# Kernel tuning notes

Measured on AMD Instinct MI355X. Metric: run time of the kernel, lower is better.

## Reference

```python
import jax, jax.numpy as jnp
import numpy as np

N = 20000      # nodes
E = 50000      # edges
B = 128        # graphs in batch
H = 64         # hidden_dim
FEAT = 28      # raw node feature dim
N_TYPES = 100  # one-hot size for node_type
EDGE_DIM = 5   # one-hot size for edge_type
OUT = 1        # output_dim
MP_ITER = 3
S2S_ITER = 4


def setup_inputs() -> dict:
    key = jax.random.key(0)
    ks = jax.random.split(key, 24)
    s = 0.05
    inp = {
        'node_feat': jax.random.normal(ks[0], (N, FEAT), dtype=jnp.float32),
        'node_type': jax.random.randint(ks[1], (N,), 0, N_TYPES),
        'edge_index': jax.random.randint(ks[2], (2, E), 0, N),
        'edge_type': jax.random.randint(ks[3], (E,), 0, EDGE_DIM),
        'batch': jnp.sort(jax.random.randint(ks[4], (N,), 0, B)),
        # node embedding
        'W_emb': jax.random.normal(ks[5], (N_TYPES + FEAT, H), dtype=jnp.float32) * s,
        'b_emb': jnp.zeros((H,), dtype=jnp.float32),
        # shared edge net: edge_dim -> H -> H*H
        'W_e1': jax.random.normal(ks[6], (EDGE_DIM, H), dtype=jnp.float32) * s,
        'b_e1': jnp.zeros((H,), dtype=jnp.float32),
        'W_e2': jax.random.normal(ks[7], (H, H * H), dtype=jnp.float32) * s,
        'b_e2': jnp.zeros((H * H,), dtype=jnp.float32),
        # per-layer NNConv root weight + bias
        'roots': jax.random.normal(ks[8], (MP_ITER, H, H), dtype=jnp.float32) * s,
        'conv_bias': jnp.zeros((MP_ITER, H), dtype=jnp.float32),
        # Set2Set LSTM (input 2H, hidden H); torch gate order i,f,g,o
        'W_ih': jax.random.normal(ks[9], (4 * H, 2 * H), dtype=jnp.float32) * s,
        'W_hh': jax.random.normal(ks[10], (4 * H, H), dtype=jnp.float32) * s,
        'b_ih': jnp.zeros((4 * H,), dtype=jnp.float32),
        'b_hh': jnp.zeros((4 * H,), dtype=jnp.float32),
        # output MLP 2H -> H -> OUT
        'W_o1': jax.random.normal(ks[11], (2 * H, H), dtype=jnp.float32) * s,
        'b_o1': jnp.zeros((H,), dtype=jnp.float32),
        'W_o2': jax.random.normal(ks[12], (H, OUT), dtype=jnp.float32) * s,
        'b_o2': jnp.zeros((OUT,), dtype=jnp.float32),
    }
    return inp


def _forward(node_feat, W_emb, b_emb, W_e1, b_e1, W_e2, b_e2, roots, conv_bias,
             W_ih, W_hh, b_ih, b_hh, W_o1, b_o1, W_o2, b_o2,
             node_type, edge_index, edge_type, batch):
    # node embedding: [one_hot(node_type,100) ; node_feat] @ W_emb
    x_in = jnp.concatenate(
        [jax.nn.one_hot(node_type, N_TYPES, dtype=node_feat.dtype), node_feat], axis=-1)
    h = x_in @ W_emb + b_emb                                   # [N, H]

    # edge-conditioned weights (edge_attr is fixed, edge_net is shared across
    # iterations, so nn(edge_attr) is identical each layer -> compute once)
    edge_attr = jax.nn.one_hot(edge_type, EDGE_DIM, dtype=node_feat.dtype)
    Wmat = jax.nn.relu(edge_attr @ W_e1 + b_e1) @ W_e2 + b_e2  # [E, H*H]
    Wmat = Wmat.reshape(E, H, H)                               # [E, H_in, H_out]

    src, dst = edge_index[0], edge_index[1]
    for i in range(MP_ITER):
        msg = jnp.einsum('eh,eho->eo', h[src], Wmat)           # per-edge matvec
        agg = jax.ops.segment_sum(msg, dst, num_segments=N)    # sum aggregation
        h = agg + h @ roots[i] + conv_bias[i]                  # NNConv root + bias

    # Set2Set pooling
    hx = jnp.zeros((B, H), dtype=h.dtype)
    cx = jnp.zeros((B, H), dtype=h.dtype)
    q_star = jnp.zeros((B, 2 * H), dtype=h.dtype)
    for _ in range(S2S_ITER):
        gates = q_star @ W_ih.T + b_ih + hx @ W_hh.T + b_hh
        ig, fg, gg, og = jnp.split(gates, 4, axis=-1)
        cx = jax.nn.sigmoid(fg) * cx + jax.nn.sigmoid(ig) * jnp.tanh(gg)
        hx = jax.nn.sigmoid(og) * jnp.tanh(cx)
        q = hx                                                 # [B, H]
        e = jnp.sum(h * q[batch], axis=-1)                     # [N]
        m = jax.lax.stop_gradient(jax.ops.segment_max(e, batch, num_segments=B))
        a = jnp.exp(e - m[batch])
        denom = jax.ops.segment_sum(a, batch, num_segments=B)
        denom = jnp.where(denom == 0, 1.0, denom)
        a = a / denom[batch]                                   # scatter softmax
        r = jax.ops.segment_sum(a[:, None] * h, batch, num_segments=B)  # [B, H]
        q_star = jnp.concatenate([q, r], axis=-1)

    out = jax.nn.relu(q_star @ W_o1 + b_o1) @ W_o2 + b_o2      # [B, OUT]
    return out


def reference(node_feat, node_type, edge_index, edge_type, batch,
              W_emb, b_emb, W_e1, b_e1, W_e2, b_e2, roots, conv_bias,
              W_ih, W_hh, b_ih, b_hh, W_o1, b_o1, W_o2, b_o2):
    return _forward(node_feat, W_emb, b_emb, W_e1, b_e1, W_e2, b_e2, roots,
                    conv_bias, W_ih, W_hh, b_ih, b_hh, W_o1, b_o1, W_o2, b_o2,
                    node_type, edge_index, edge_type, batch)
```

## Files before the change

### kernel.cpp

```cpp
#include <hip/hip_runtime.h>
#include <math.h>


#define NN 20000
#define NE 50000
#define NB 128
#define HD 64
#define NFEAT 28
#define NTYPES 100
#define EDIM 5
#define MPIT 3
#define S2SIT 4
#define NBLK_E ((NE + 255) / 256)
#define SMAX 224
#define HP (HD + 1)

__device__ __forceinline__ float sigm(float x) {
  return 1.0f / (1.0f + expf(-x));
}

__global__ __launch_bounds__(256) void k_starts(
    const int* __restrict__ batch, int* __restrict__ gstart) {
  int n = blockIdx.x * blockDim.x + threadIdx.x;
  if (n >= NN) return;
  int b = batch[n];
  if (n == 0)
    for (int t = 0; t <= b; ++t) gstart[t] = 0;
  int bn = (n + 1 < NN) ? batch[n + 1] : NB;
  for (int t = b + 1; t <= bn; ++t) gstart[t] = n + 1;
}

__global__ __launch_bounds__(256) void k_setup(
    const float* __restrict__ feat, const int* __restrict__ ntype,
    const int* __restrict__ etype,
    const float* __restrict__ W_emb, const float* __restrict__ b_emb,
    const float* __restrict__ W_e1, const float* __restrict__ b_e1,
    const float* __restrict__ W_e2, const float* __restrict__ b_e2,
    const float* __restrict__ W_ih, const float* __restrict__ W_hh,
    float* __restrict__ Wty, float* __restrict__ hA, float* __restrict__ hB,
    float* __restrict__ W_ihT, float* __restrict__ W_hhT,
    int* __restrict__ bc) {
  __shared__ int wcc[4][EDIM];
  __shared__ float sv[EDIM][HD];
  __shared__ float red[4][EDIM][HD];
  const int tid = threadIdx.x;
  const int lane = tid & 63;
  const int wv = tid >> 6;
  const int blk = blockIdx.x;
  const int nblk = gridDim.x;
  const int nthr = nblk << 8;
  const int gtid = (blk << 8) + tid;
  const int gw = (blk << 2) + wv;
  const int nwave = nblk << 2;

  if (blk < NBLK_E) {
    int e = (blk << 8) + tid;
    int ty = (e < NE) ? etype[e] : -1;
    #pragma unroll
    for (int t = 0; t < EDIM; ++t) {
      unsigned long long m = __ballot(ty == t);
      if (lane == 0) wcc[wv][t] = __popcll(m);
    }
    __syncthreads();
    if (tid < EDIM)
      bc[blk * EDIM + tid] = wcc[0][tid] + wcc[1][tid] + wcc[2][tid] + wcc[3][tid];
    __syncthreads();
  }

  if (blk >= NBLK_E && blk < NBLK_E + 64) {
    int mbase = (blk - NBLK_E) * 64;
    for (int idx = tid; idx < EDIM * HD; idx += 256) {
      int t = idx >> 6, j = idx & 63;
      float x = W_e1[t * HD + j] + b_e1[j];
      sv[t][j] = x > 0.f ? x : 0.f;
    }
    __syncthreads();
    int l = tid & 63, jg = tid >> 6;
    float acc[EDIM] = {0.f, 0.f, 0.f, 0.f, 0.f};
    #pragma unroll
    for (int jj = 0; jj < 16; ++jj) {
      int j = jg * 16 + jj;
      float w2 = W_e2[j * 4096 + mbase + l];
      #pragma unroll
      for (int t = 0; t < EDIM; ++t) acc[t] = fmaf(sv[t][j], w2, acc[t]);
    }
    #pragma unroll
    for (int t = 0; t < EDIM; ++t) red[jg][t][l] = acc[t];
    __syncthreads();
    for (int idx = tid; idx < EDIM * HD; idx += 256) {
      int t = idx >> 6, m = idx & 63;
      float s = red[0][t][m] + red[1][t][m] + red[2][t][m] + red[3][t][m];
      Wty[t * 4096 + mbase + m] = s + b_e2[mbase + m];
    }
  }

  for (int o = gtid; o < 2 * HD * 4 * HD; o += nthr)
    W_ihT[o] = W_ih[(o & 255) * 128 + (o >> 8)];
  for (int o = gtid; o < HD * 4 * HD; o += nthr)
    W_hhT[o] = W_hh[(o & 255) * 64 + (o >> 8)];

  {
    float wf[NFEAT];
    #pragma unroll
    for (int f = 0; f < NFEAT; ++f) wf[f] = W_emb[(NTYPES + f) * HD + lane];
    float bb = b_emb[lane];
    for (int n = gw; n < NN; n += nwave) {
      int nu = __builtin_amdgcn_readfirstlane(n);
      int t = __builtin_amdgcn_readfirstlane(ntype[nu]);
      const float* row = feat + nu * NFEAT;
      float acc = bb + W_emb[t * HD + lane];
      #pragma unroll
      for (int f = 0; f < NFEAT; ++f) acc = fmaf(row[f], wf[f], acc);
      hA[nu * HD + lane] = acc;
    }
  }

  {
    float4 z = make_float4(0.f, 0.f, 0.f, 0.f);
    for (int i = gtid; i < NN * HD / 4; i += nthr)
      reinterpret_cast<float4*>(hB)[i] = z;
  }
}

__global__ __launch_bounds__(256) void k_place(
    const int* __restrict__ etype, const int* __restrict__ ei,
    const int* __restrict__ bc,
    int* __restrict__ srcs, int* __restrict__ dsts, int* __restrict__ offs_out) {
  __shared__ int s_base[EDIM];
  __shared__ int wc[4][EDIM];
  const int tid = threadIdx.x;
  const int lane = tid & 63;
  const int wv = tid >> 6;
  const int blk = blockIdx.x;

  if (wv == 0) {
    int part[EDIM], tot[EDIM];
    #pragma unroll
    for (int t = 0; t < EDIM; ++t) { part[t] = 0; tot[t] = 0; }
    for (int b = lane; b < NBLK_E; b += 64) {
      #pragma unroll
      for (int t = 0; t < EDIM; ++t) {
        int x = bc[b * EDIM + t];
        tot[t] += x;
        if (b < blk) part[t] += x;
      }
    }
    #pragma unroll
    for (int t = 0; t < EDIM; ++t) {
      #pragma unroll
      for (int off = 32; off; off >>= 1) {
        tot[t]  += __shfl_xor(tot[t],  off, 64);
        part[t] += __shfl_xor(part[t], off, 64);
      }
    }
    if (lane == 0) {
      int run = 0;
      #pragma unroll
      for (int t = 0; t < EDIM; ++t) {
        s_base[t] = run + part[t];
        if (blk == 0) offs_out[t] = run;
        run += tot[t];
      }
      if (blk == 0) offs_out[EDIM] = run;
    }
  }

  int e = (blk << 8) + tid;
  int ty = (e < NE) ? etype[e] : -1;
  int sv = 0, dv = 0;
  if (e < NE) { sv = ei[e]; dv = ei[NE + e]; }
  int rank = 0;
  #pragma unroll
  for (int t = 0; t < EDIM; ++t) {
    unsigned long long m = __ballot(ty == t);
    if (lane == 0) wc[wv][t] = __popcll(m);
    if (ty == t) rank = __popcll(m & ((1ull << lane) - 1ull));
  }
  __syncthreads();
  if (ty >= 0) {
    int base = s_base[ty];
    for (int w = 0; w < wv; ++w) base += wc[w][ty];
    srcs[base + rank] = sv;
    dsts[base + rank] = dv;
  }
}

__global__ __launch_bounds__(256) void k_mp(
    const int* __restrict__ srcs, const int* __restrict__ dsts,
    const int* __restrict__ offs_in,
    const float* __restrict__ Wty, const float* __restrict__ hsrc,
    float* __restrict__ htgt, float* __restrict__ hzero,
    const float* __restrict__ root, const float* __restrict__ bias) {
  const int lane = threadIdx.x & 63;
  const int wv = threadIdx.x >> 6;
  const int blk = blockIdx.x;

  if (blk < 512) {
    float w[HD];
    #pragma unroll
    for (int k = 0; k < HD; ++k) w[k] = root[k * HD + lane];
    float bb = bias[lane];
    int rw = (blk << 2) + wv;
    for (int n = rw; n < NN; n += 2048) {
      int nu = __builtin_amdgcn_readfirstlane(n);
      const float* row = hsrc + nu * HD;
      float a0 = bb, a1 = 0.f, a2 = 0.f, a3 = 0.f;
      #pragma unroll
      for (int k = 0; k < HD; k += 4) {
        a0 = fmaf(row[k + 0], w[k + 0], a0);
        a1 = fmaf(row[k + 1], w[k + 1], a1);
        a2 = fmaf(row[k + 2], w[k + 2], a2);
        a3 = fmaf(row[k + 3], w[k + 3], a3);
      }
      atomicAdd(&htgt[nu * HD + lane], (a0 + a1) + (a2 + a3));
    }
    if (hzero) {
      float4 z = make_float4(0.f, 0.f, 0.f, 0.f);
      for (int i = (blk << 8) + threadIdx.x; i < NN * HD / 4; i += 512 * 256)
        reinterpret_cast<float4*>(hzero)[i] = z;
    }
  } else {
    int wid = ((blk - 512) << 2) + wv;
    const int nw = 8192;
    int per = (NE + nw - 1) / nw;
    int beg = wid * per;
    int end = beg + per; if (end > NE) end = NE;
    if (beg >= end) return;
    int offs[EDIM + 1];
    #pragma unroll
    for (int t = 0; t <= EDIM; ++t) offs[t] = offs_in[t];
    for (int t = 0; t < EDIM; ++t) {
      int lo = offs[t];     if (lo < beg) lo = beg;
      int hi = offs[t + 1]; if (hi > end) hi = end;
      if (lo >= hi) continue;
      float w[HD];
      #pragma unroll
      for (int k = 0; k < HD; ++k) w[k] = Wty[t * 4096 + k * HD + lane];
      for (int p = lo; p < hi; ++p) {
        int s = __builtin_amdgcn_readfirstlane(srcs[p]);
        int d = __builtin_amdgcn_readfirstlane(dsts[p]);
        const float* row = hsrc + s * HD;
        float a0 = 0.f, a1 = 0.f, a2 = 0.f, a3 = 0.f;
        #pragma unroll
        for (int k = 0; k < HD; k += 4) {
          a0 = fmaf(row[k + 0], w[k + 0], a0);
          a1 = fmaf(row[k + 1], w[k + 1], a1);
          a2 = fmaf(row[k + 2], w[k + 2], a2);
          a3 = fmaf(row[k + 3], w[k + 3], a3);
        }
        atomicAdd(&htgt[d * HD + lane], (a0 + a1) + (a2 + a3));
      }
    }
  }
}

__global__ __launch_bounds__(256) void k_s2s(
    const float* __restrict__ h, const int* __restrict__ gstart,
    const float* __restrict__ W_ihT, const float* __restrict__ W_hhT,
    const float* __restrict__ b_ih, const float* __restrict__ b_hh,
    const float* __restrict__ W_o1, const float* __restrict__ b_o1,
    const float* __restrict__ W_o2, const float* __restrict__ b_o2,
    float* __restrict__ out) {
  __shared__ float hs[SMAX * HP];
  __shared__ float ebuf[SMAX];
  __shared__ float qstar[2 * HD];
  __shared__ float hxs[HD], cxs[HD], gates[4 * HD];
  __shared__ float redM[4], redS[4], redR[4][HD];
  __shared__ float hid[HD];
  int b = blockIdx.x;
  int tid = threadIdx.x;
  int lane = tid & 63, wv = tid >> 6;

  int st = gstart[b], en = gstart[b + 1];
  int cnt = en - st;
  int cached = cnt < SMAX ? cnt : SMAX;

  int total = cached * HD;
  for (int base = tid * 4; base < total; base += 1024) {
    float4 v = *reinterpret_cast<const float4*>(h + st * HD + base);
    int n = base >> 6, k = base & 63;
    float* row = hs + n * HP + k;
    row[0] = v.x; row[1] = v.y; row[2] = v.z; row[3] = v.w;
  }
  if (tid < 2 * HD) qstar[tid] = 0.f;
  if (tid < HD) { hxs[tid] = 0.f; cxs[tid] = 0.f; }
  __syncthreads();

  for (int it = 0; it < S2SIT; ++it) {
    float acc0 = b_ih[tid] + b_hh[tid], acc1 = 0.f;
    #pragma unroll 8
    for (int j = 0; j < 2 * HD; j += 2) {
      acc0 = fmaf(qstar[j],     W_ihT[j * 256 + tid],       acc0);
      acc1 = fmaf(qstar[j + 1], W_ihT[(j + 1) * 256 + tid], acc1);
    }
    #pragma unroll 8
    for (int j = 0; j < HD; j += 2) {
      acc0 = fmaf(hxs[j],     W_hhT[j * 256 + tid],       acc0);
      acc1 = fmaf(hxs[j + 1], W_hhT[(j + 1) * 256 + tid], acc1);
    }
    gates[tid] = acc0 + acc1;
    __syncthreads();
    if (tid < HD) {
      float ig = sigm(gates[tid]);
      float fg = sigm(gates[HD + tid]);
      float gg = tanhf(gates[2 * HD + tid]);
      float og = sigm(gates[3 * HD + tid]);
      float c = fmaf(fg, cxs[tid], ig * gg);
      cxs[tid] = c;
      hxs[tid] = og * tanhf(c);
    }
    __syncthreads();

    float e = -1e30f;
    if (tid < cached) {
      const float* row = hs + tid * HP;
      float d0 = 0.f, d1 = 0.f;
      #pragma unroll 8
      for (int k = 0; k < HD; k += 2) {
        d0 = fmaf(row[k],     hxs[k],     d0);
        d1 = fmaf(row[k + 1], hxs[k + 1], d1);
      }
      e = d0 + d1;
      ebuf[tid] = e;
    }
    float m = e;
    #pragma unroll
    for (int off = 32; off; off >>= 1) m = fmaxf(m, __shfl_xor(m, off, 64));
    float qreg = hxs[lane];
    for (int n = cached + wv; n < cnt; n += 4) {
      float ev = h[(st + n) * HD + lane] * qreg;
      #pragma unroll
      for (int off = 32; off; off >>= 1) ev += __shfl_xor(ev, off, 64);
      m = fmaxf(m, ev);
    }
    if (lane == 0) redM[wv] = m;
    __syncthreads();
    float M = fmaxf(fmaxf(redM[0], redM[1]), fmaxf(redM[2], redM[3]));

    float sp = 0.f;
    if (tid < cached) {
      float a = expf(ebuf[tid] - M);
      ebuf[tid] = a;
      sp = a;
    }
    #pragma unroll
    for (int off = 32; off; off >>= 1) sp += __shfl_xor(sp, off, 64);
    __syncthreads();

    float r = 0.f;
    for (int n = wv; n < cached; n += 4)
      r = fmaf(ebuf[n], hs[n * HP + lane], r);
    float s_tail = 0.f;
    for (int n = cached + wv; n < cnt; n += 4) {
      float v = h[(st + n) * HD + lane];
      float ev = v * qreg;
      #pragma unroll
      for (int off = 32; off; off >>= 1) ev += __shfl_xor(ev, off, 64);
      float a = expf(ev - M);
      s_tail += a;
      r = fmaf(a, v, r);
    }
    if (lane == 0) redS[wv] = sp + s_tail;
    redR[wv][lane] = r;
    __syncthreads();
    if (tid < HD) {
      float S = redS[0] + redS[1] + redS[2] + redS[3];
      float R = redR[0][tid] + redR[1][tid] + redR[2][tid] + redR[3][tid];
      if (S == 0.f) S = 1.f;
      qstar[tid] = hxs[tid];
      qstar[HD + tid] = R / S;
    }
    __syncthreads();
  }

  if (tid < HD) {
    float acc = b_o1[tid];
    #pragma unroll 8
    for (int i = 0; i < 2 * HD; ++i)
      acc = fmaf(qstar[i], W_o1[i * HD + tid], acc);
    hid[tid] = acc > 0.f ? acc : 0.f;
  }
  __syncthreads();
  if (tid < HD) {
    float p = hid[tid] * W_o2[tid];
    #pragma unroll
    for (int off = 32; off; off >>= 1) p += __shfl_xor(p, off, 64);
    if (tid == 0) out[b] = p + b_o2[0];
  }
}

extern "C" void kernel_launch(void* const* d_in, const int* in_sizes, int n_in,
                              void* d_out, int out_size, void* d_ws, size_t ws_size,
                              hipStream_t stream) {
  const float* node_feat = (const float*)d_in[0];
  const int*   node_type = (const int*)d_in[1];
  const int*   edge_index= (const int*)d_in[2];
  const int*   edge_type = (const int*)d_in[3];
  const int*   batch     = (const int*)d_in[4];
  const float* W_emb     = (const float*)d_in[5];
  const float* b_emb     = (const float*)d_in[6];
  const float* W_e1      = (const float*)d_in[7];
  const float* b_e1      = (const float*)d_in[8];
  const float* W_e2      = (const float*)d_in[9];
  const float* b_e2      = (const float*)d_in[10];
  const float* roots     = (const float*)d_in[11];
  const float* conv_bias = (const float*)d_in[12];
  const float* W_ih      = (const float*)d_in[13];
  const float* W_hh      = (const float*)d_in[14];
  const float* b_ih      = (const float*)d_in[15];
  const float* b_hh      = (const float*)d_in[16];
  const float* W_o1      = (const float*)d_in[17];
  const float* b_o1      = (const float*)d_in[18];
  const float* W_o2      = (const float*)d_in[19];
  const float* b_o2      = (const float*)d_in[20];
  float* out = (float*)d_out;

  float* Wty   = (float*)d_ws;
  float* hA    = Wty + EDIM * 4096;
  float* hB    = hA + NN * HD;
  float* hC    = hB + NN * HD;
  float* W_ihT = hC + NN * HD;
  float* W_hhT = W_ihT + 2 * HD * 4 * HD;
  int*   srcs  = (int*)(W_hhT + HD * 4 * HD);
  int*   dsts  = srcs + NE;
  int*   gstart= dsts + NE;
  int*   bc    = gstart + 136;
  int*   offs  = bc + NBLK_E * EDIM;

  k_starts<<<(NN + 255) / 256, 256, 0, stream>>>(batch, gstart);
  k_setup<<<512, 256, 0, stream>>>(node_feat, node_type, edge_type,
                                   W_emb, b_emb, W_e1, b_e1, W_e2, b_e2,
                                   W_ih, W_hh, Wty, hA, hB, W_ihT, W_hhT, bc);
  k_place<<<NBLK_E, 256, 0, stream>>>(edge_type, edge_index, bc, srcs, dsts, offs);

  k_mp<<<2560, 256, 0, stream>>>(srcs, dsts, offs, Wty, hA, hB, hC,
                                 roots + 0 * HD * HD, conv_bias + 0 * HD);
  k_mp<<<2560, 256, 0, stream>>>(srcs, dsts, offs, Wty, hB, hC, hA,
                                 roots + 1 * HD * HD, conv_bias + 1 * HD);
  k_mp<<<2560, 256, 0, stream>>>(srcs, dsts, offs, Wty, hC, hA, (float*)0,
                                 roots + 2 * HD * HD, conv_bias + 2 * HD);

  k_s2s<<<NB, 256, 0, stream>>>(hA, gstart, W_ihT, W_hhT, b_ih, b_hh,
                                W_o1, b_o1, W_o2, b_o2, out);
}
```

Measured before the change: 208.9 us.

## Split message passing into root-store and edge-atomic kernels, drop zero-fill buffer

Replaces the fused per-layer kernel with two launches per layer. The first is a root-transform kernel that writes bias plus h·root directly with plain stores. The second is an edge-message kernel that atomically accumulates into that same buffer. This removes the separate zero-fill passes and the third ping-pong buffer, avoids atomics on the root contribution, and packs src/dst into int2 for a single load per edge. In exchange there are three extra kernel launches, and the root and edge work are serialized within each layer instead of running concurrently.

```diff
diff --git a/kernel.cpp b/kernel.cpp
--- a/kernel.cpp
+++ b/kernel.cpp
@@ -37,7 +37,7 @@
     const float* __restrict__ W_e1, const float* __restrict__ b_e1,
     const float* __restrict__ W_e2, const float* __restrict__ b_e2,
     const float* __restrict__ W_ih, const float* __restrict__ W_hh,
-    float* __restrict__ Wty, float* __restrict__ hA, float* __restrict__ hB,
+    float* __restrict__ Wty, float* __restrict__ hA,
     float* __restrict__ W_ihT, float* __restrict__ W_hhT,
     int* __restrict__ bc) {
   __shared__ int wcc[4][EDIM];
@@ -114,18 +114,12 @@
       hA[nu * HD + lane] = acc;
     }
   }
-
-  {
-    float4 z = make_float4(0.f, 0.f, 0.f, 0.f);
-    for (int i = gtid; i < NN * HD / 4; i += nthr)
-      reinterpret_cast<float4*>(hB)[i] = z;
-  }
 }
 
 __global__ __launch_bounds__(256) void k_place(
     const int* __restrict__ etype, const int* __restrict__ ei,
     const int* __restrict__ bc,
-    int* __restrict__ srcs, int* __restrict__ dsts, int* __restrict__ offs_out) {
+    int2* __restrict__ sd, int* __restrict__ offs_out) {
   __shared__ int s_base[EDIM];
   __shared__ int wc[4][EDIM];
   const int tid = threadIdx.x;
@@ -180,31 +174,62 @@
   if (ty >= 0) {
     int base = s_base[ty];
     for (int w = 0; w < wv; ++w) base += wc[w][ty];
-    srcs[base + rank] = sv;
-    dsts[base + rank] = dv;
-  }
-}
-
-__global__ __launch_bounds__(256) void k_mp(
-    const int* __restrict__ srcs, const int* __restrict__ dsts,
-    const int* __restrict__ offs_in,
-    const float* __restrict__ Wty, const float* __restrict__ hsrc,
-    float* __restrict__ htgt, float* __restrict__ hzero,
+    sd[base + rank] = make_int2(sv, dv);
+  }
+}
+
+__global__ __launch_bounds__(256) void k_root(
+    const float* __restrict__ h, float* __restrict__ hnext,
     const float* __restrict__ root, const float* __restrict__ bias) {
   const int lane = threadIdx.x & 63;
+  const int wid = __builtin_amdgcn_readfirstlane(blockIdx.x * 4 + (threadIdx.x >> 6));
+  const int nw = gridDim.x * 4;
+  float w[HD];
+  #pragma unroll
+  for (int k = 0; k < HD; ++k) w[k] = root[k * HD + lane];
+  float bb = bias[lane];
+  for (int n = wid; n < NN; n += nw) {
+    const float* row = h + n * HD;
+    float a0 = 0.f, a1 = 0.f, a2 = 0.f, a3 = 0.f;
+    #pragma unroll
+    for (int k = 0; k < HD; k += 4) {
+      a0 = fmaf(row[k + 0], w[k + 0], a0);
+      a1 = fmaf(row[k + 1], w[k + 1], a1);
+      a2 = fmaf(row[k + 2], w[k + 2], a2);
+      a3 = fmaf(row[k + 3], w[k + 3], a3);
+    }
+    hnext[n * HD + lane] = bb + ((a0 + a1) + (a2 + a3));
+  }
+}
+
+__global__ __launch_bounds__(256) void k_msg(
+    const int2* __restrict__ sd, const int* __restrict__ offs_in,
+    const float* __restrict__ Wty, const float* __restrict__ hsrc,
+    float* __restrict__ htgt) {
+  const int lane = threadIdx.x & 63;
   const int wv = threadIdx.x >> 6;
-  const int blk = blockIdx.x;
-
-  if (blk < 512) {
+  int wid = (blockIdx.x << 2) + wv;
+  const int nw = 8192;
+  int per = (NE + nw - 1) / nw;
+  int beg = wid * per;
+  int end = beg + per; if (end > NE) end = NE;
+  if (beg >= end) return;
+  int offs[EDIM + 1];
+  #pragma unroll
+  for (int t = 0; t <= EDIM; ++t) offs[t] = offs_in[t];
+  for (int t = 0; t < EDIM; ++t) {
+    int lo = offs[t];     if (lo < beg) lo = beg;
+    int hi = offs[t + 1]; if (hi > end) hi = end;
+    if (lo >= hi) continue;
     float w[HD];
     #pragma unroll
-    for (int k = 0; k < HD; ++k) w[k] = root[k * HD + lane];
-    float bb = bias[lane];
-    int rw = (blk << 2) + wv;
-    for (int n = rw; n < NN; n += 2048) {
-      int nu = __builtin_amdgcn_readfirstlane(n);
-      const float* row = hsrc + nu * HD;
-      float a0 = bb, a1 = 0.f, a2 = 0.f, a3 = 0.f;
+    for (int k = 0; k < HD; ++k) w[k] = Wty[t * 4096 + k * HD + lane];
+    for (int p = lo; p < hi; ++p) {
+      int2 e = sd[p];
+      int s = __builtin_amdgcn_readfirstlane(e.x);
+      int d = __builtin_amdgcn_readfirstlane(e.y);
+      const float* row = hsrc + s * HD;
+      float a0 = 0.f, a1 = 0.f, a2 = 0.f, a3 = 0.f;
       #pragma unroll
       for (int k = 0; k < HD; k += 4) {
         a0 = fmaf(row[k + 0], w[k + 0], a0);
@@ -212,44 +237,7 @@
         a2 = fmaf(row[k + 2], w[k + 2], a2);
         a3 = fmaf(row[k + 3], w[k + 3], a3);
       }
-      atomicAdd(&htgt[nu * HD + lane], (a0 + a1) + (a2 + a3));
-    }
-    if (hzero) {
-      float4 z = make_float4(0.f, 0.f, 0.f, 0.f);
-      for (int i = (blk << 8) + threadIdx.x; i < NN * HD / 4; i += 512 * 256)
-        reinterpret_cast<float4*>(hzero)[i] = z;
-    }
-  } else {
-    int wid = ((blk - 512) << 2) + wv;
-    const int nw = 8192;
-    int per = (NE + nw - 1) / nw;
-    int beg = wid * per;
-    int end = beg + per; if (end > NE) end = NE;
-    if (beg >= end) return;
-    int offs[EDIM + 1];
-    #pragma unroll
-    for (int t = 0; t <= EDIM; ++t) offs[t] = offs_in[t];
-    for (int t = 0; t < EDIM; ++t) {
-      int lo = offs[t];     if (lo < beg) lo = beg;
-      int hi = offs[t + 1]; if (hi > end) hi = end;
-      if (lo >= hi) continue;
-      float w[HD];
-      #pragma unroll
-      for (int k = 0; k < HD; ++k) w[k] = Wty[t * 4096 + k * HD + lane];
-      for (int p = lo; p < hi; ++p) {
-        int s = __builtin_amdgcn_readfirstlane(srcs[p]);
-        int d = __builtin_amdgcn_readfirstlane(dsts[p]);
-        const float* row = hsrc + s * HD;
-        float a0 = 0.f, a1 = 0.f, a2 = 0.f, a3 = 0.f;
-        #pragma unroll
-        for (int k = 0; k < HD; k += 4) {
-          a0 = fmaf(row[k + 0], w[k + 0], a0);
-          a1 = fmaf(row[k + 1], w[k + 1], a1);
-          a2 = fmaf(row[k + 2], w[k + 2], a2);
-          a3 = fmaf(row[k + 3], w[k + 3], a3);
-        }
-        atomicAdd(&htgt[d * HD + lane], (a0 + a1) + (a2 + a3));
-      }
+      atomicAdd(&htgt[d * HD + lane], (a0 + a1) + (a2 + a3));
     }
   }
 }
@@ -418,28 +406,28 @@
   float* Wty   = (float*)d_ws;
   float* hA    = Wty + EDIM * 4096;
   float* hB    = hA + NN * HD;
-  float* hC    = hB + NN * HD;
-  float* W_ihT = hC + NN * HD;
+  float* W_ihT = hB + NN * HD;
   float* W_hhT = W_ihT + 2 * HD * 4 * HD;
-  int*   srcs  = (int*)(W_hhT + HD * 4 * HD);
-  int*   dsts  = srcs + NE;
-  int*   gstart= dsts + NE;
+  int2*  sd    = (int2*)(W_hhT + HD * 4 * HD);
+  int*   gstart= (int*)(sd + NE);
   int*   bc    = gstart + 136;
   int*   offs  = bc + NBLK_E * EDIM;
 
   k_starts<<<(NN + 255) / 256, 256, 0, stream>>>(batch, gstart);
   k_setup<<<512, 256, 0, stream>>>(node_feat, node_type, edge_type,
                                    W_emb, b_emb, W_e1, b_e1, W_e2, b_e2,
-                                   W_ih, W_hh, Wty, hA, hB, W_ihT, W_hhT, bc);
-  k_place<<<NBLK_E, 256, 0, stream>>>(edge_type, edge_index, bc, srcs, dsts, offs);
-
-  k_mp<<<2560, 256, 0, stream>>>(srcs, dsts, offs, Wty, hA, hB, hC,
-                                 roots + 0 * HD * HD, conv_bias + 0 * HD);
-  k_mp<<<2560, 256, 0, stream>>>(srcs, dsts, offs, Wty, hB, hC, hA,
-                                 roots + 1 * HD * HD, conv_bias + 1 * HD);
-  k_mp<<<2560, 256, 0, stream>>>(srcs, dsts, offs, Wty, hC, hA, (float*)0,
-                                 roots + 2 * HD * HD, conv_bias + 2 * HD);
-
-  k_s2s<<<NB, 256, 0, stream>>>(hA, gstart, W_ihT, W_hhT, b_ih, b_hh,
+                                   W_ih, W_hh, Wty, hA, W_ihT, W_hhT, bc);
+  k_place<<<NBLK_E, 256, 0, stream>>>(edge_type, edge_index, bc, sd, offs);
+
+  const float* hcur = hA;
+  float* hnxt = hB;
+  for (int i = 0; i < MPIT; ++i) {
+    k_root<<<512, 256, 0, stream>>>(hcur, hnxt, roots + i * HD * HD,
+                                    conv_bias + i * HD);
+    k_msg<<<2048, 256, 0, stream>>>(sd, offs, Wty, hcur, hnxt);
+    const float* tmp = hnxt; hnxt = (float*)hcur; hcur = tmp;
+  }
+
+  k_s2s<<<NB, 256, 0, stream>>>(hcur, gstart, W_ihT, W_hhT, b_ih, b_hh,
                                 W_o1, b_o1, W_o2, b_o2, out);
 }
```

Result: slower. 240.2 us (+15.0%).

## Pack edge src/dst/type into int2 and prefetch source rows per wave

Applied to the files above, without the earlier changes.

Edge placement now writes a single int2 per edge holding the source index, the edge type in the upper bits and the destination, so the separate offsets array goes away. Each edge wave handles a fixed 7 edges. It loads all of their descriptors with one vector load and prefetches every source row as a coalesced per-lane load. The matvec then broadcasts row elements with readlane instead of scalar loads from global memory, and reloads the type weight only when the type changes. The aim is to raise memory-level parallelism on the gathers. The cost is more readlane instructions and a 16-bit limit on source indices.

```diff
diff --git a/kernel.cpp b/kernel.cpp
--- a/kernel.cpp
+++ b/kernel.cpp
@@ -14,9 +14,14 @@
 #define NBLK_E ((NE + 255) / 256)
 #define SMAX 224
 #define HP (HD + 1)
+#define EPW 7
 
 __device__ __forceinline__ float sigm(float x) {
   return 1.0f / (1.0f + expf(-x));
+}
+
+__device__ __forceinline__ float rdlane(float v, int l) {
+  return __uint_as_float(__builtin_amdgcn_readlane(__float_as_uint(v), l));
 }
 
 __global__ __launch_bounds__(256) void k_starts(
@@ -124,8 +129,7 @@
 
 __global__ __launch_bounds__(256) void k_place(
     const int* __restrict__ etype, const int* __restrict__ ei,
-    const int* __restrict__ bc,
-    int* __restrict__ srcs, int* __restrict__ dsts, int* __restrict__ offs_out) {
+    const int* __restrict__ bc, int2* __restrict__ sd) {
   __shared__ int s_base[EDIM];
   __shared__ int wc[4][EDIM];
   const int tid = threadIdx.x;
@@ -158,10 +162,8 @@
       #pragma unroll
       for (int t = 0; t < EDIM; ++t) {
         s_base[t] = run + part[t];
-        if (blk == 0) offs_out[t] = run;
         run += tot[t];
       }
-      if (blk == 0) offs_out[EDIM] = run;
     }
   }
 
@@ -180,14 +182,12 @@
   if (ty >= 0) {
     int base = s_base[ty];
     for (int w = 0; w < wv; ++w) base += wc[w][ty];
-    srcs[base + rank] = sv;
-    dsts[base + rank] = dv;
+    sd[base + rank] = make_int2(sv | (ty << 16), dv);
   }
 }
 
 __global__ __launch_bounds__(256) void k_mp(
-    const int* __restrict__ srcs, const int* __restrict__ dsts,
-    const int* __restrict__ offs_in,
+    const int2* __restrict__ sd,
     const float* __restrict__ Wty, const float* __restrict__ hsrc,
     float* __restrict__ htgt, float* __restrict__ hzero,
     const float* __restrict__ root, const float* __restrict__ bias) {
@@ -221,35 +221,41 @@
     }
   } else {
     int wid = ((blk - 512) << 2) + wv;
-    const int nw = 8192;
-    int per = (NE + nw - 1) / nw;
-    int beg = wid * per;
-    int end = beg + per; if (end > NE) end = NE;
-    if (beg >= end) return;
-    int offs[EDIM + 1];
-    #pragma unroll
-    for (int t = 0; t <= EDIM; ++t) offs[t] = offs_in[t];
-    for (int t = 0; t < EDIM; ++t) {
-      int lo = offs[t];     if (lo < beg) lo = beg;
-      int hi = offs[t + 1]; if (hi > end) hi = end;
-      if (lo >= hi) continue;
-      float w[HD];
-      #pragma unroll
-      for (int k = 0; k < HD; ++k) w[k] = Wty[t * 4096 + k * HD + lane];
-      for (int p = lo; p < hi; ++p) {
-        int s = __builtin_amdgcn_readfirstlane(srcs[p]);
-        int d = __builtin_amdgcn_readfirstlane(dsts[p]);
-        const float* row = hsrc + s * HD;
-        float a0 = 0.f, a1 = 0.f, a2 = 0.f, a3 = 0.f;
+    int beg = wid * EPW;
+    if (beg >= NE) return;
+    int len = NE - beg; if (len > EPW) len = EPW;
+
+    int2 ed = sd[beg + (lane < len ? lane : len - 1)];
+
+    float hv[EPW];
+    #pragma unroll
+    for (int j = 0; j < EPW; ++j) {
+      int sx = __builtin_amdgcn_readlane(ed.x, j < EPW ? j : 0);
+      hv[j] = hsrc[(sx & 0xFFFF) * HD + lane];
+    }
+
+    int curt = -1;
+    float w[HD];
+    #pragma unroll
+    for (int j = 0; j < EPW; ++j) {
+      if (j >= len) break;
+      int ex = __builtin_amdgcn_readlane(ed.x, j);
+      int dj = __builtin_amdgcn_readlane(ed.y, j);
+      int ty = ex >> 16;
+      if (ty != curt) {
+        curt = ty;
         #pragma unroll
-        for (int k = 0; k < HD; k += 4) {
-          a0 = fmaf(row[k + 0], w[k + 0], a0);
-          a1 = fmaf(row[k + 1], w[k + 1], a1);
-          a2 = fmaf(row[k + 2], w[k + 2], a2);
-          a3 = fmaf(row[k + 3], w[k + 3], a3);
-        }
-        atomicAdd(&htgt[d * HD + lane], (a0 + a1) + (a2 + a3));
-      }
+        for (int k = 0; k < HD; ++k) w[k] = Wty[ty * 4096 + k * HD + lane];
+      }
+      float a0 = 0.f, a1 = 0.f, a2 = 0.f, a3 = 0.f;
+      #pragma unroll
+      for (int k = 0; k < HD; k += 4) {
+        a0 = fmaf(rdlane(hv[j], k + 0), w[k + 0], a0);
+        a1 = fmaf(rdlane(hv[j], k + 1), w[k + 1], a1);
+        a2 = fmaf(rdlane(hv[j], k + 2), w[k + 2], a2);
+        a3 = fmaf(rdlane(hv[j], k + 3), w[k + 3], a3);
+      }
+      atomicAdd(&htgt[dj * HD + lane], (a0 + a1) + (a2 + a3));
     }
   }
 }
@@ -421,23 +427,21 @@
   float* hC    = hB + NN * HD;
   float* W_ihT = hC + NN * HD;
   float* W_hhT = W_ihT + 2 * HD * 4 * HD;
-  int*   srcs  = (int*)(W_hhT + HD * 4 * HD);
-  int*   dsts  = srcs + NE;
-  int*   gstart= dsts + NE;
+  int2*  sd    = (int2*)(W_hhT + HD * 4 * HD);
+  int*   gstart= (int*)(sd + NE);
   int*   bc    = gstart + 136;
-  int*   offs  = bc + NBLK_E * EDIM;
 
   k_starts<<<(NN + 255) / 256, 256, 0, stream>>>(batch, gstart);
   k_setup<<<512, 256, 0, stream>>>(node_feat, node_type, edge_type,
                                    W_emb, b_emb, W_e1, b_e1, W_e2, b_e2,
                                    W_ih, W_hh, Wty, hA, hB, W_ihT, W_hhT, bc);
-  k_place<<<NBLK_E, 256, 0, stream>>>(edge_type, edge_index, bc, srcs, dsts, offs);
-
-  k_mp<<<2560, 256, 0, stream>>>(srcs, dsts, offs, Wty, hA, hB, hC,
+  k_place<<<NBLK_E, 256, 0, stream>>>(edge_type, edge_index, bc, sd);
+
+  k_mp<<<2560, 256, 0, stream>>>(sd, Wty, hA, hB, hC,
                                  roots + 0 * HD * HD, conv_bias + 0 * HD);
-  k_mp<<<2560, 256, 0, stream>>>(srcs, dsts, offs, Wty, hB, hC, hA,
+  k_mp<<<2560, 256, 0, stream>>>(sd, Wty, hB, hC, hA,
                                  roots + 1 * HD * HD, conv_bias + 1 * HD);
-  k_mp<<<2560, 256, 0, stream>>>(srcs, dsts, offs, Wty, hC, hA, (float*)0,
+  k_mp<<<2560, 256, 0, stream>>>(sd, Wty, hC, hA, (float*)0,
                                  roots + 2 * HD * HD, conv_bias + 2 * HD);
 
   k_s2s<<<NB, 256, 0, stream>>>(hA, gstart, W_ihT, W_hhT, b_ih, b_hh,
```

Result: no change. 207.3 us (-0.8%).
